# Kernel optimization log

Measured on AMD Instinct MI355X. Metric: run time of the kernel, lower is better.

Reference implementation:

```python
import jax, jax.numpy as jnp
import numpy as np

TEMP = 0.5
EPS = 1e-8  # torch CosineSimilarity eps


def setup_inputs() -> dict:
    key = jax.random.key(0)
    k1, k2 = jax.random.split(key)
    B, D = 4096, 512
    z_i = jax.random.normal(k1, (B, D), dtype=jnp.float32)
    z_j = jax.random.normal(k2, (B, D), dtype=jnp.float32)
    return {"z_i": z_i, "z_j": z_j}


def reference(z_i, z_j):
    B = z_i.shape[0]
    N = 2 * B
    z = jnp.concatenate([z_i, z_j], axis=0)              # [N, D]
    norm = jnp.maximum(jnp.linalg.norm(z, axis=1, keepdims=True), EPS)
    zn = z / norm                                        # unit rows
    sim = jnp.matmul(zn, zn.T) / TEMP                    # [N, N] cosine sims / temperature
    # positives: sim[i, i+B] for i<B and sim[i+B, i] for i<B
    pos = jnp.concatenate([jnp.diagonal(sim, offset=B), jnp.diagonal(sim, offset=-B)])  # [N]
    # CE over logits [pos, negatives] with label 0 == -pos + logsumexp(row without diagonal)
    diag_mask = jnp.eye(N, dtype=bool)
    sim_masked = jnp.where(diag_mask, -jnp.inf, sim)
    lse = jax.nn.logsumexp(sim_masked, axis=1)           # [N]
    loss = jnp.sum(lse - pos) / N                        # CrossEntropyLoss(reduction='sum') / N
    return loss
```

## Files before the change

### kernel.cpp

```cpp
#include <hip/hip_runtime.h>
#include <stdint.h>

#define NROWS 8192
#define HALF_N 4096
#define DIM 512
#define INV_TEMP 2.0f
#define E2SCALE 2.8853900817779268f
#define LN2 0.6931471805599453f
#define NTILES 2080

typedef int i32x8 __attribute__((ext_vector_type(8)));
typedef float f32x16 __attribute__((ext_vector_type(16)));

__device__ __forceinline__ void gload_lds16(const unsigned char* g, unsigned char* l) {
  __builtin_amdgcn_global_load_lds(
      (const __attribute__((address_space(1))) unsigned int*)(uintptr_t)g,
      (__attribute__((address_space(3))) unsigned int*)(uint32_t)(uintptr_t)l,
      16, 0, 0);
}

__global__ void __launch_bounds__(256) k_normalize(const float* __restrict__ zi,
                                                   const float* __restrict__ zj,
                                                   unsigned char* __restrict__ zn,
                                                   float* __restrict__ sumexp) {
  int tid = threadIdx.x;
  int gid = blockIdx.x * 256 + tid;
  if (gid < NROWS) sumexp[gid] = 0.0f;
  int wave = tid >> 6, lane = tid & 63;
  int row = blockIdx.x * 4 + wave;
  const float* src = (row < HALF_N) ? (zi + (size_t)row * DIM)
                                    : (zj + (size_t)(row - HALF_N) * DIM);
  const float4* s4 = (const float4*)src;
  float4 a = s4[lane];
  float4 b = s4[lane + 64];
  float ss = a.x * a.x + a.y * a.y + a.z * a.z + a.w * a.w +
             b.x * b.x + b.y * b.y + b.z * b.z + b.w * b.w;
#pragma unroll
  for (int off = 32; off > 0; off >>= 1) ss += __shfl_xor(ss, off, 64);
  float inv = 1.0f / fmaxf(sqrtf(ss), 1e-8f);
  int w0 = __builtin_amdgcn_cvt_pk_fp8_f32(a.x * inv, a.y * inv, 0, false);
  w0 = __builtin_amdgcn_cvt_pk_fp8_f32(a.z * inv, a.w * inv, w0, true);
  int w1 = __builtin_amdgcn_cvt_pk_fp8_f32(b.x * inv, b.y * inv, 0, false);
  w1 = __builtin_amdgcn_cvt_pk_fp8_f32(b.z * inv, b.w * inv, w1, true);
  unsigned char* dst = zn + (size_t)row * DIM;
  *((int*)(dst + lane * 4)) = w0;
  *((int*)(dst + 256 + lane * 4)) = w1;
}

__global__ void __launch_bounds__(256) k_simsum(const unsigned char* __restrict__ zn,
                                                float* __restrict__ sumexp,
                                                float* __restrict__ posv) {
  __shared__ __align__(16) unsigned char As[2][128 * 64];
  __shared__ __align__(16) unsigned char Bs[2][128 * 64];
  int tid = threadIdx.x;
  int wave = tid >> 6, lane = tid & 63;

  int idx = blockIdx.x;
  int tn = (int)((sqrtf(8.0f * idx + 1.0f) - 1.0f) * 0.5f);
  while (tn * (tn + 1) / 2 > idx) tn--;
  while ((tn + 1) * (tn + 2) / 2 <= idx) tn++;
  int tm = idx - tn * (tn + 1) / 2;
  int rowBase = tm * 128, colBase = tn * 128;
  int wr = (wave >> 1) * 64, wc = (wave & 1) * 64;
  int h = lane >> 5, c32 = lane & 31;

  int rA = wave * 32 + (lane >> 2);
  int chunk = (lane & 3) ^ ((rA >> 1) & 3);
  const unsigned char* gA = zn + (size_t)(rowBase + rA) * DIM + chunk * 16;
  const unsigned char* gB = zn + (size_t)(colBase + rA) * DIM + chunk * 16;
  unsigned char* lA[2] = {&As[0][wave * 2048], &As[1][wave * 2048]};
  unsigned char* lB[2] = {&Bs[0][wave * 2048], &Bs[1][wave * 2048]};

#define STAGE(b)                                  \
  do {                                            \
    gload_lds16(gA, lA[b]);                       \
    gload_lds16(gA + 16 * DIM, lA[b] + 1024);     \
    gload_lds16(gB, lB[b]);                       \
    gload_lds16(gB + 16 * DIM, lB[b] + 1024);     \
    gA += 64; gB += 64;                           \
  } while (0)

  f32x16 acc[2][2];
#pragma unroll
  for (int i = 0; i < 2; i++)
#pragma unroll
    for (int j = 0; j < 2; j++)
#pragma unroll
      for (int r = 0; r < 16; r++) acc[i][j][r] = 0.f;

  int sg = (c32 >> 1) & 3;
  int p0 = (2 * h) ^ sg, p1 = p0 ^ 1;
  int aIdx[2] = {(wr + c32) * 4, (wr + 32 + c32) * 4};
  int bIdx[2] = {(wc + c32) * 4, (wc + 32 + c32) * 4};

#define COMPUTE(b)                                                                   \
  do {                                                                               \
    const int4* Av = (const int4*)As[b];                                             \
    const int4* Bv = (const int4*)Bs[b];                                             \
    i32x8 af[2], bfr[2];                                                             \
    _Pragma("unroll") for (int i = 0; i < 2; i++) {                                  \
      int4 lo = Av[aIdx[i] + p0], hi = Av[aIdx[i] + p1];                             \
      af[i] = (i32x8){lo.x, lo.y, lo.z, lo.w, hi.x, hi.y, hi.z, hi.w};               \
    }                                                                                \
    _Pragma("unroll") for (int j = 0; j < 2; j++) {                                  \
      int4 lo = Bv[bIdx[j] + p0], hi = Bv[bIdx[j] + p1];                             \
      bfr[j] = (i32x8){lo.x, lo.y, lo.z, lo.w, hi.x, hi.y, hi.z, hi.w};              \
    }                                                                                \
    _Pragma("unroll") for (int i = 0; i < 2; i++)                                    \
      _Pragma("unroll") for (int j = 0; j < 2; j++)                                  \
        acc[i][j] = __builtin_amdgcn_mfma_scale_f32_32x32x64_f8f6f4(                 \
            af[i], bfr[j], acc[i][j], 0, 0,                               \
            0, 0x7F, 0, 0x7F);                                     \
  } while (0)

  STAGE(0);
#pragma unroll
  for (int s = 0; s < 8; s += 2) {
    __syncthreads();
    if (s + 1 < 8) STAGE(1);
    COMPUTE(0);
    __syncthreads();
    if (s + 2 < 8) STAGE(0);
    COMPUTE(1);
  }

  bool isDiag = (tm == tn);
  bool hasPos = (tn == tm + 32);
  bool diagLane = (wr == wc) && (h == ((c32 >> 2) & 1));
  int rsel = (c32 & 3) | ((c32 >> 3) << 2);

  if (isDiag && diagLane) {
    acc[0][0][rsel] = -1e30f;
    acc[1][1][rsel] = -1e30f;
  }
  if (hasPos && diagLane) {
#pragma unroll
    for (int i = 0; i < 2; i++) {
      float sv = acc[i][i][rsel] * INV_TEMP;
      int gr = rowBase + wr + i * 32 + c32;
      posv[gr] = sv;
      posv[gr + HALF_N] = sv;
    }
  }

  float rp[32], cp[2] = {0.f, 0.f};
#pragma unroll
  for (int i = 0; i < 2; i++)
#pragma unroll
    for (int r = 0; r < 16; r++) {
      float e0 = __builtin_amdgcn_exp2f(acc[i][0][r] * E2SCALE);
      float e1 = __builtin_amdgcn_exp2f(acc[i][1][r] * E2SCALE);
      rp[i * 16 + r] = e0 + e1;
      cp[0] += e0;
      cp[1] += e1;
    }

#pragma unroll
  for (int t = 0; t < 16; t++) {
    float mine = (lane & 16) ? rp[t + 16] : rp[t];
    float oth = __shfl_xor((lane & 16) ? rp[t] : rp[t + 16], 16, 64);
    rp[t] = mine + oth;
  }
#pragma unroll
  for (int t = 0; t < 8; t++) {
    float mine = (lane & 8) ? rp[t + 8] : rp[t];
    float oth = __shfl_xor((lane & 8) ? rp[t] : rp[t + 8], 8, 64);
    rp[t] = mine + oth;
  }
#pragma unroll
  for (int t = 0; t < 4; t++) {
    float mine = (lane & 4) ? rp[t + 4] : rp[t];
    float oth = __shfl_xor((lane & 4) ? rp[t] : rp[t + 4], 4, 64);
    rp[t] = mine + oth;
  }
#pragma unroll
  for (int t = 0; t < 2; t++) {
    float mine = (lane & 2) ? rp[t + 2] : rp[t];
    float oth = __shfl_xor((lane & 2) ? rp[t] : rp[t + 2], 2, 64);
    rp[t] = mine + oth;
  }
  {
    float mine = (lane & 1) ? rp[1] : rp[0];
    float oth = __shfl_xor((lane & 1) ? rp[0] : rp[1], 1, 64);
    rp[0] = mine + oth;
  }
  int myrow = rowBase + wr + 32 * (c32 >> 4) + (c32 & 3) + 8 * ((c32 >> 2) & 3) + 4 * h;
  atomicAdd(&sumexp[myrow], rp[0]);

  if (!isDiag) {
    cp[0] += __shfl_xor(cp[0], 32, 64);
    cp[1] += __shfl_xor(cp[1], 32, 64);
    float cv = h ? cp[1] : cp[0];
    atomicAdd(&sumexp[colBase + wc + h * 32 + c32], cv);
  }
#undef STAGE
#undef COMPUTE
}

__global__ void __launch_bounds__(1024) k_final(const float* __restrict__ sumexp,
                                                const float* __restrict__ posv,
                                                float* __restrict__ out) {
  __shared__ float red[16];
  int tid = threadIdx.x;
  const float4* se4 = (const float4*)sumexp;
  const float4* pv4 = (const float4*)posv;
  float p = 0.f;
#pragma unroll
  for (int c = 0; c < 2; c++) {
    float4 se = se4[tid * 2 + c];
    float4 pv = pv4[tid * 2 + c];
    p += (__builtin_amdgcn_logf(se.x) + __builtin_amdgcn_logf(se.y) +
          __builtin_amdgcn_logf(se.z) + __builtin_amdgcn_logf(se.w)) * LN2 -
         (pv.x + pv.y + pv.z + pv.w);
  }
#pragma unroll
  for (int off = 32; off > 0; off >>= 1) p += __shfl_xor(p, off, 64);
  int wv = tid >> 6, ln = tid & 63;
  if (ln == 0) red[wv] = p;
  __syncthreads();
  if (tid == 0) {
    float t = 0.f;
    for (int w = 0; w < 16; w++) t += red[w];
    out[0] = t / (float)NROWS;
  }
}

extern "C" void kernel_launch(void* const* d_in, const int* in_sizes, int n_in,
                              void* d_out, int out_size, void* d_ws, size_t ws_size,
                              hipStream_t stream) {
  const float* zi = (const float*)d_in[0];
  const float* zj = (const float*)d_in[1];
  unsigned char* zn = (unsigned char*)d_ws;
  float* sumexp = (float*)((char*)d_ws + (size_t)NROWS * DIM);
  float* posv = sumexp + NROWS;
  float* out = (float*)d_out;

  hipLaunchKernelGGL(k_normalize, dim3(2048), dim3(256), 0, stream, zi, zj, zn, sumexp);
  hipLaunchKernelGGL(k_simsum, dim3(NTILES), dim3(256), 0, stream, zn, sumexp, posv);
  hipLaunchKernelGGL(k_final, dim3(1), dim3(1024), 0, stream, sumexp, posv, out);
}
```

Baseline: 96.44 us.

## Load MFMA operands directly from global memory, dropping LDS staging

Measured after the change: 134.3 us. 39.3% more time.

```diff
diff --git a/kernel.cpp b/kernel.cpp
--- a/kernel.cpp
+++ b/kernel.cpp
@@ -11,13 +11,6 @@
 
 typedef int i32x8 __attribute__((ext_vector_type(8)));
 typedef float f32x16 __attribute__((ext_vector_type(16)));
-
-__device__ __forceinline__ void gload_lds16(const unsigned char* g, unsigned char* l) {
-  __builtin_amdgcn_global_load_lds(
-      (const __attribute__((address_space(1))) unsigned int*)(uintptr_t)g,
-      (__attribute__((address_space(3))) unsigned int*)(uint32_t)(uintptr_t)l,
-      16, 0, 0);
-}
 
 __global__ void __launch_bounds__(256) k_normalize(const float* __restrict__ zi,
                                                    const float* __restrict__ zj,
@@ -50,8 +43,6 @@
 __global__ void __launch_bounds__(256) k_simsum(const unsigned char* __restrict__ zn,
                                                 float* __restrict__ sumexp,
                                                 float* __restrict__ posv) {
-  __shared__ __align__(16) unsigned char As[2][128 * 64];
-  __shared__ __align__(16) unsigned char Bs[2][128 * 64];
   int tid = threadIdx.x;
   int wave = tid >> 6, lane = tid & 63;
 
@@ -64,21 +55,10 @@
   int wr = (wave >> 1) * 64, wc = (wave & 1) * 64;
   int h = lane >> 5, c32 = lane & 31;
 
-  int rA = wave * 32 + (lane >> 2);
-  int chunk = (lane & 3) ^ ((rA >> 1) & 3);
-  const unsigned char* gA = zn + (size_t)(rowBase + rA) * DIM + chunk * 16;
-  const unsigned char* gB = zn + (size_t)(colBase + rA) * DIM + chunk * 16;
-  unsigned char* lA[2] = {&As[0][wave * 2048], &As[1][wave * 2048]};
-  unsigned char* lB[2] = {&Bs[0][wave * 2048], &Bs[1][wave * 2048]};
-
-#define STAGE(b)                                  \
-  do {                                            \
-    gload_lds16(gA, lA[b]);                       \
-    gload_lds16(gA + 16 * DIM, lA[b] + 1024);     \
-    gload_lds16(gB, lB[b]);                       \
-    gload_lds16(gB + 16 * DIM, lB[b] + 1024);     \
-    gA += 64; gB += 64;                           \
-  } while (0)
+  const unsigned char* A0 = zn + (size_t)(rowBase + wr + c32) * DIM + h * 32;
+  const unsigned char* A1 = A0 + 32 * DIM;
+  const unsigned char* B0 = zn + (size_t)(colBase + wc + c32) * DIM + h * 32;
+  const unsigned char* B1 = B0 + 32 * DIM;
 
   f32x16 acc[2][2];
 #pragma unroll
@@ -88,41 +68,30 @@
 #pragma unroll
       for (int r = 0; r < 16; r++) acc[i][j][r] = 0.f;
 
-  int sg = (c32 >> 1) & 3;
-  int p0 = (2 * h) ^ sg, p1 = p0 ^ 1;
-  int aIdx[2] = {(wr + c32) * 4, (wr + 32 + c32) * 4};
-  int bIdx[2] = {(wc + c32) * 4, (wc + 32 + c32) * 4};
-
-#define COMPUTE(b)                                                                   \
-  do {                                                                               \
-    const int4* Av = (const int4*)As[b];                                             \
-    const int4* Bv = (const int4*)Bs[b];                                             \
-    i32x8 af[2], bfr[2];                                                             \
-    _Pragma("unroll") for (int i = 0; i < 2; i++) {                                  \
-      int4 lo = Av[aIdx[i] + p0], hi = Av[aIdx[i] + p1];                             \
-      af[i] = (i32x8){lo.x, lo.y, lo.z, lo.w, hi.x, hi.y, hi.z, hi.w};               \
-    }                                                                                \
-    _Pragma("unroll") for (int j = 0; j < 2; j++) {                                  \
-      int4 lo = Bv[bIdx[j] + p0], hi = Bv[bIdx[j] + p1];                             \
-      bfr[j] = (i32x8){lo.x, lo.y, lo.z, lo.w, hi.x, hi.y, hi.z, hi.w};              \
-    }                                                                                \
-    _Pragma("unroll") for (int i = 0; i < 2; i++)                                    \
-      _Pragma("unroll") for (int j = 0; j < 2; j++)                                  \
-        acc[i][j] = __builtin_amdgcn_mfma_scale_f32_32x32x64_f8f6f4(                 \
-            af[i], bfr[j], acc[i][j], 0, 0,                               \
-            0, 0x7F, 0, 0x7F);                                     \
-  } while (0)
-
-  STAGE(0);
-#pragma unroll
-  for (int s = 0; s < 8; s += 2) {
-    __syncthreads();
-    if (s + 1 < 8) STAGE(1);
-    COMPUTE(0);
-    __syncthreads();
-    if (s + 2 < 8) STAGE(0);
-    COMPUTE(1);
-  }
+#define LD8(p, off)                                                        \
+  ({                                                                       \
+    int4 lo = *(const int4*)((p) + (off));                                 \
+    int4 hi = *(const int4*)((p) + (off) + 16);                            \
+    (i32x8){lo.x, lo.y, lo.z, lo.w, hi.x, hi.y, hi.z, hi.w};               \
+  })
+
+#pragma unroll
+  for (int s = 0; s < 8; s++) {
+    int o = s * 64;
+    i32x8 a0 = LD8(A0, o);
+    i32x8 a1 = LD8(A1, o);
+    i32x8 b0 = LD8(B0, o);
+    i32x8 b1 = LD8(B1, o);
+    acc[0][0] = __builtin_amdgcn_mfma_scale_f32_32x32x64_f8f6f4(a0, b0, acc[0][0],
+                                                                0, 0, 0, 0x7F, 0, 0x7F);
+    acc[0][1] = __builtin_amdgcn_mfma_scale_f32_32x32x64_f8f6f4(a0, b1, acc[0][1],
+                                                                0, 0, 0, 0x7F, 0, 0x7F);
+    acc[1][0] = __builtin_amdgcn_mfma_scale_f32_32x32x64_f8f6f4(a1, b0, acc[1][0],
+                                                                0, 0, 0, 0x7F, 0, 0x7F);
+    acc[1][1] = __builtin_amdgcn_mfma_scale_f32_32x32x64_f8f6f4(a1, b1, acc[1][1],
+                                                                0, 0, 0, 0x7F, 0, 0x7F);
+  }
+#undef LD8
 
   bool isDiag = (tm == tn);
   bool hasPos = (tn == tm + 32);
@@ -193,8 +162,6 @@
     float cv = h ? cp[1] : cp[0];
     atomicAdd(&sumexp[colBase + wc + h * 32 + c32], cv);
   }
-#undef STAGE
-#undef COMPUTE
 }
 
 __global__ void __launch_bounds__(1024) k_final(const float* __restrict__ sumexp,
```
